# Kernel tuning notes

Hardware: AMD Instinct MI355X
Metric: run time of the kernel (lower is better)

## Reference

```python
import jax, jax.numpy as jnp
import numpy as np

B, N, NS, D, H = 32, 4096, 16, 512, 8
DH = D // H          # dims_per_head = 64
DFF = 4 * D          # ff_mlp hidden
SCALE = DH ** -0.5
EPS = 1e-8           # slot-attention renorm eps
LN_EPS = 1e-5        # torch LayerNorm default
ITERS = 3


def layer_norm(x, g, b):
    mu = jnp.mean(x, axis=-1, keepdims=True)
    var = jnp.mean((x - mu) ** 2, axis=-1, keepdims=True)
    return (x - mu) * jax.lax.rsqrt(var + LN_EPS) * g + b


def setup_inputs() -> dict:
    key = jax.random.key(0)
    ks = jax.random.split(key, 8)
    s = 0.02
    return {
        "inputs": jax.random.normal(ks[0], (B, N, D), jnp.float32),
        "conditioning": jax.random.normal(ks[1], (B, NS, D), jnp.float32),
        # norm_input
        "ln_in_g": jnp.ones((D,), jnp.float32),
        "ln_in_b": jnp.zeros((D,), jnp.float32),
        # projections (no bias: use_projection_bias=False)
        "Wk": jax.random.normal(ks[2], (D, D), jnp.float32) * s,
        "Wv": jax.random.normal(ks[3], (D, D), jnp.float32) * s,
        "Wq": jax.random.normal(ks[4], (D, D), jnp.float32) * s,
        "Wo": jax.random.normal(ks[5], (D, D), jnp.float32) * s,
        # norm_slots / norm_slots_ff_mlp
        "ln_s_g": jnp.ones((D,), jnp.float32),
        "ln_s_b": jnp.zeros((D,), jnp.float32),
        "ln_f_g": jnp.ones((D,), jnp.float32),
        "ln_f_b": jnp.zeros((D,), jnp.float32),
        # ff_mlp: Linear(D,4D) -> ReLU -> Linear(4D,D)
        "W1": jax.random.normal(ks[6], (D, DFF), jnp.float32) * s,
        "b1": jnp.zeros((DFF,), jnp.float32),
        "W2": jax.random.normal(ks[7], (DFF, D), jnp.float32) * s,
        "b2": jnp.zeros((D,), jnp.float32),
    }


def reference(inputs, conditioning, ln_in_g, ln_in_b, Wk, Wv, Wq, Wo,
              ln_s_g, ln_s_b, ln_f_g, ln_f_b, W1, b1, W2, b2):
    b = inputs.shape[0]
    x = layer_norm(inputs, ln_in_g, ln_in_b)                 # [b, n, D]
    k = (x @ Wk.T).reshape(b, N, H, DH)                      # [b, n, h, dh]
    v = (x @ Wv.T).reshape(b, N, H, DH)

    slots = conditioning
    attn_mean = None
    for _ in range(ITERS):
        slots_prev = slots
        s = layer_norm(slots, ln_s_g, ln_s_b)
        q = (s @ Wq.T).reshape(b, NS, H, DH)                 # [b, ns, h, dh]
        dots = jnp.einsum("bihd,bjhd->bihj", q, k) * SCALE   # [b, ns, h, n]
        # softmax over flattened (slots, heads) axis, per input location j
        attn = jax.nn.softmax(dots.reshape(b, NS * H, N), axis=1)
        attn = attn.reshape(b, NS, H, N)
        attn_before = attn
        attn = attn + EPS
        attn = attn / jnp.sum(attn, axis=-1, keepdims=True)  # renorm over j
        updates = jnp.einsum("bjhd,bihj->bihd", v, attn)     # [b, ns, h, dh]
        updates = updates.reshape(b, NS, D)
        slots = updates @ Wo.T + slots_prev                  # to_o + residual
        slots_prev_ff = slots
        s2 = layer_norm(slots, ln_f_g, ln_f_b)
        s2 = jax.nn.relu(s2 @ W1 + b1) @ W2 + b2             # ff_mlp
        slots = s2 + slots_prev_ff
        attn_mean = jnp.mean(attn_before, axis=2)            # [b, ns, n]
    return slots, attn_mean
```

## Files before the change

kernel.cpp:

```cpp
#include <hip/hip_runtime.h>
#include <cstdint>
#include <cstddef>

typedef __attribute__((ext_vector_type(8))) short short8;
typedef __attribute__((ext_vector_type(4))) short short4v;
typedef __attribute__((ext_vector_type(8))) __bf16 bf16x8;
typedef __attribute__((ext_vector_type(4))) float f32x4;
typedef unsigned short u16;

static constexpr int Bb = 32, Nn = 4096, NSs = 16, Dd = 512, Hh = 8, DFF = 2048;
static constexpr float SCALE = 0.125f;
static constexpr float EPSR  = 1e-8f;
static constexpr float LN_EPS = 1e-5f;
static constexpr int JS = 16;

__device__ __forceinline__ u16 f2b(float x) {
  union { float f; uint32_t u; } a; a.f = x;
  uint32_t r = a.u + 0x7fffu + ((a.u >> 16) & 1u);
  return (u16)(r >> 16);
}
__device__ __forceinline__ float b2f(u16 x) {
  union { uint32_t u; float f; } a; a.u = ((uint32_t)x) << 16; return a.f;
}

__device__ __forceinline__ f32x4 mfma16(short8 a, short8 b, f32x4 c) {
  return __builtin_amdgcn_mfma_f32_16x16x32_bf16(
      __builtin_bit_cast(bf16x8, a), __builtin_bit_cast(bf16x8, b), c, 0, 0, 0);
}

__device__ __forceinline__ void gload16(const u16* g, u16* l) {
  __builtin_amdgcn_global_load_lds(
      (const __attribute__((address_space(1))) void*)g,
      (__attribute__((address_space(3))) void*)l, 16, 0, 0);
}

__global__ __launch_bounds__(256) void ln_rows(const float* __restrict__ src,
    const float* __restrict__ g, const float* __restrict__ bt,
    u16* __restrict__ dst, int R) {
  int row = blockIdx.x * 4 + (threadIdx.x >> 6);
  if (row >= R) return;
  int lane = threadIdx.x & 63;
  const float* p = src + (size_t)row * Dd + lane * 8;
  float4 u0 = *(const float4*)p;
  float4 u1 = *(const float4*)(p + 4);
  float x[8] = {u0.x,u0.y,u0.z,u0.w,u1.x,u1.y,u1.z,u1.w};
  float s = 0.f, s2 = 0.f;
#pragma unroll
  for (int e = 0; e < 8; ++e) { s += x[e]; s2 += x[e]*x[e]; }
#pragma unroll
  for (int m = 1; m < 64; m <<= 1) { s += __shfl_xor(s, m); s2 += __shfl_xor(s2, m); }
  float mean = s * (1.f/512.f);
  float var  = s2 * (1.f/512.f) - mean*mean;
  float rstd = rsqrtf(var + LN_EPS);
  union { u16 o[8]; short8 v; } ou;
#pragma unroll
  for (int e = 0; e < 8; ++e)
    ou.o[e] = f2b((x[e]-mean)*rstd*g[lane*8+e] + bt[lane*8+e]);
  *(short8*)(dst + (size_t)row * Dd + lane * 8) = ou.v;
}

__global__ __launch_bounds__(256, 2) void gemm_kv(const u16* __restrict__ A,
    const u16* __restrict__ Bk, const u16* __restrict__ Bv,
    u16* __restrict__ Ck, u16* __restrict__ CvT) {
  __shared__ u16 lA[128*64];
  __shared__ u16 lK[128*64];
  __shared__ u16 lV[128*64];
  const int tid = threadIdx.x, lane = tid & 63, wid = tid >> 6;
  const int wr = wid >> 1, wc = wid & 1;
  const int n  = blockIdx.y * 4 + blockIdx.x;
  const int orig = (n & 7) * 512 + (n >> 3);
  const int bm = (orig >> 2) * 128, bn = (orig & 3) * 128;
  const size_t BN = (size_t)Bb * Nn;
  f32x4 ak[4][4] = {};
  f32x4 av[4][4] = {};
  const int sr = lane >> 3;
  const int ss = ((lane & 7) ^ (sr & 7)) * 8;
  const int li = lane & 15, lk = lane >> 4;
  const int sx = (li & 7) * 8;
  for (int t = 0; t < 8; ++t) {
    const int k0 = t * 64;
    __syncthreads();
#pragma unroll
    for (int gi = 0; gi < 4; ++gi) {
      const int rb = wid * 32 + gi * 8;
      gload16(A  + (size_t)(bm + rb + sr) * Dd + k0 + ss, &lA[rb * 64]);
      gload16(Bk + (size_t)(bn + rb + sr) * Dd + k0 + ss, &lK[rb * 64]);
      gload16(Bv + (size_t)(bn + rb + sr) * Dd + k0 + ss, &lV[rb * 64]);
    }
    __syncthreads();
#pragma unroll
    for (int kk = 0; kk < 2; ++kk) {
      const int cs = ((kk * 4 + lk) * 8) ^ sx;
      short8 af[4], kf[4], vf[4];
#pragma unroll
      for (int m = 0; m < 4; ++m)
        af[m] = *(const short8*)&lA[(wr*64 + m*16 + li)*64 + cs];
#pragma unroll
      for (int nn2 = 0; nn2 < 4; ++nn2) {
        kf[nn2] = *(const short8*)&lK[(wc*64 + nn2*16 + li)*64 + cs];
        vf[nn2] = *(const short8*)&lV[(wc*64 + nn2*16 + li)*64 + cs];
      }
#pragma unroll
      for (int m = 0; m < 4; ++m)
#pragma unroll
        for (int nn2 = 0; nn2 < 4; ++nn2) {
          ak[m][nn2] = mfma16(kf[nn2], af[m], ak[m][nn2]);
          av[m][nn2] = mfma16(af[m], vf[nn2], av[m][nn2]);
        }
    }
  }
#pragma unroll
  for (int m = 0; m < 4; ++m)
#pragma unroll
    for (int nn2 = 0; nn2 < 4; ++nn2) {
      {
        int row = bm + wr*64 + m*16 + li;
        int c0  = bn + wc*64 + nn2*16 + lk*4;
        f32x4 vk = ak[m][nn2];
        union { u16 o[4]; short4v v4; } ou;
#pragma unroll
        for (int r = 0; r < 4; ++r) ou.o[r] = f2b(vk[r]);
        *(short4v*)&Ck[(size_t)row * Dd + c0] = ou.v4;
      }
      {
        int col = bn + wc*64 + nn2*16 + li;
        int r0  = bm + wr*64 + m*16 + lk*4;
        f32x4 vv = av[m][nn2];
        union { u16 o[4]; short4v v4; } ou;
#pragma unroll
        for (int r = 0; r < 4; ++r) ou.o[r] = f2b(vv[r]);
        *(short4v*)&CvT[(size_t)col * BN + r0] = ou.v4;
      }
    }
}

template<int EP>
__global__ __launch_bounds__(256) void gemm64(const u16* __restrict__ A,
    const u16* __restrict__ Bw, void* __restrict__ Cp,
    const float* __restrict__ bias, const float* __restrict__ res,
    int N, int K) {
  const int lane = threadIdx.x & 63, wid = threadIdx.x >> 6;
  const int wr = wid >> 1, wc = wid & 1;
  const int bm = blockIdx.y * 64, bn = blockIdx.x * 64;
  const int li = lane & 15, lk = lane >> 4;
  f32x4 acc[2][2] = {};
  const u16* Ap = A  + (size_t)(bm + wr*32 + li) * K + lk*8;
  const u16* Bp = Bw + (size_t)(bn + wc*32 + li) * K + lk*8;
#pragma unroll 4
  for (int k0 = 0; k0 < K; k0 += 32) {
    short8 af[2], bf[2];
    af[0] = *(const short8*)(Ap + k0);
    af[1] = *(const short8*)(Ap + (size_t)16*K + k0);
    bf[0] = *(const short8*)(Bp + k0);
    bf[1] = *(const short8*)(Bp + (size_t)16*K + k0);
#pragma unroll
    for (int m = 0; m < 2; ++m)
#pragma unroll
      for (int nn2 = 0; nn2 < 2; ++nn2)
        acc[m][nn2] = mfma16(bf[nn2], af[m], acc[m][nn2]);
  }
#pragma unroll
  for (int m = 0; m < 2; ++m)
#pragma unroll
    for (int nn2 = 0; nn2 < 2; ++nn2) {
      int row = bm + wr*32 + m*16 + li;
      int c0  = bn + wc*32 + nn2*16 + lk*4;
      size_t off = (size_t)row * N + c0;
      f32x4 v = acc[m][nn2];
      if constexpr (EP == 0) {
        union { u16 o[4]; short4v v4; } ou;
#pragma unroll
        for (int r = 0; r < 4; ++r) ou.o[r] = f2b(v[r]);
        *(short4v*)&((u16*)Cp)[off] = ou.v4;
      } else if constexpr (EP == 1) {
        float4 rr = *(const float4*)&res[off];
        float4 o = {v[0] + rr.x, v[1] + rr.y, v[2] + rr.z, v[3] + rr.w};
        *(float4*)&((float*)Cp)[off] = o;
      } else if constexpr (EP == 2) {
        float4 bb = *(const float4*)&bias[c0];
        union { u16 o[4]; short4v v4; } ou;
        float x0 = v[0] + bb.x, x1 = v[1] + bb.y, x2 = v[2] + bb.z, x3 = v[3] + bb.w;
        ou.o[0] = f2b(x0 > 0.f ? x0 : 0.f); ou.o[1] = f2b(x1 > 0.f ? x1 : 0.f);
        ou.o[2] = f2b(x2 > 0.f ? x2 : 0.f); ou.o[3] = f2b(x3 > 0.f ? x3 : 0.f);
        *(short4v*)&((u16*)Cp)[off] = ou.v4;
      } else {
        float4 bb = *(const float4*)&bias[c0];
        float4 rr = *(const float4*)&res[off];
        float4 o = {v[0] + bb.x + rr.x, v[1] + bb.y + rr.y,
                    v[2] + bb.z + rr.z, v[3] + bb.w + rr.w};
        *(float4*)&((float*)Cp)[off] = o;
      }
    }
}

__global__ __launch_bounds__(512, 4) void attn_f(const u16* __restrict__ q,
    const u16* __restrict__ kk, const u16* __restrict__ vT,
    float* __restrict__ rowsum, float* __restrict__ Tpart,
    float* __restrict__ attn_mean) {
  const int js = blockIdx.x, b = blockIdx.y;
  const int tid = threadIdx.x, lane = tid & 63, h = tid >> 6;
  __shared__ float redM[8][64];
  __shared__ float redS[8][64];
  __shared__ u16 P2[8][16][72];
  const int li = lane & 15, lk = lane >> 4;
  const size_t BN = (size_t)Bb * Nn;
  const u16* qb = q + (((size_t)b*16 + li)*8 + h)*64 + lk*8;
  short8 a0 = *(const short8*)qb;
  short8 a1 = *(const short8*)(qb + 32);
  f32x4 apv[4] = {};
  float rs_acc[4] = {0.f, 0.f, 0.f, 0.f};
  for (int t2 = 0; t2 < 4; ++t2) {
    const int j0 = js * 256 + t2 * 64;
    f32x4 dt[4];
#pragma unroll
    for (int n = 0; n < 4; ++n) {
      const u16* kb = kk + ((size_t)b*Nn + j0 + n*16 + li)*Dd + h*64 + lk*8;
      f32x4 acc = {};
      acc = mfma16(a0, *(const short8*)kb, acc);
      acc = mfma16(a1, *(const short8*)(kb + 32), acc);
#pragma unroll
      for (int r = 0; r < 4; ++r) dt[n][r] = acc[r] * SCALE;
    }
#pragma unroll
    for (int n = 0; n < 4; ++n) {
      float v = fmaxf(fmaxf(dt[n][0], dt[n][1]), fmaxf(dt[n][2], dt[n][3]));
      v = fmaxf(v, __shfl_xor(v, 16));
      v = fmaxf(v, __shfl_xor(v, 32));
      if (lk == 0) redM[h][n*16 + li] = v;
    }
    __syncthreads();
    float M[4];
#pragma unroll
    for (int n = 0; n < 4; ++n) {
      float m2 = redM[0][n*16 + li];
#pragma unroll
      for (int p = 1; p < 8; ++p) m2 = fmaxf(m2, redM[p][n*16 + li]);
      M[n] = m2;
    }
#pragma unroll
    for (int n = 0; n < 4; ++n) {
      float s = 0.f;
#pragma unroll
      for (int r = 0; r < 4; ++r) { dt[n][r] = __expf(dt[n][r] - M[n]); s += dt[n][r]; }
      s += __shfl_xor(s, 16);
      s += __shfl_xor(s, 32);
      if (lk == 0) redS[h][n*16 + li] = s;
    }
    __syncthreads();
#pragma unroll
    for (int n = 0; n < 4; ++n) {
      float s2 = redS[0][n*16 + li];
#pragma unroll
      for (int p = 1; p < 8; ++p) s2 += redS[p][n*16 + li];
      float inv = 1.f / s2;
#pragma unroll
      for (int r = 0; r < 4; ++r) dt[n][r] = dt[n][r] * inv + EPSR;
    }
#pragma unroll
    for (int n = 0; n < 4; ++n)
#pragma unroll
      for (int r = 0; r < 4; ++r)
        P2[h][lk*4 + r][n*16 + li] = f2b(dt[n][r]);
#pragma unroll
    for (int r = 0; r < 4; ++r) {
      float v = dt[0][r] + dt[1][r] + dt[2][r] + dt[3][r];
      v += __shfl_xor(v, 1); v += __shfl_xor(v, 2);
      v += __shfl_xor(v, 4); v += __shfl_xor(v, 8);
      rs_acc[r] += v;
    }
    short8 pa0 = *(const short8*)&P2[h][li][lk*8];
    short8 pa1 = *(const short8*)&P2[h][li][32 + lk*8];
#pragma unroll
    for (int n = 0; n < 4; ++n) {
      const u16* vb = vT + (size_t)(h*64 + n*16 + li)*BN + (size_t)b*Nn + j0 + lk*8;
      apv[n] = mfma16(*(const short8*)vb, pa0, apv[n]);
      apv[n] = mfma16(*(const short8*)(vb + 32), pa1, apv[n]);
    }
    if (attn_mean != nullptr) {
      __syncthreads();
      int j = tid & 63;
#pragma unroll
      for (int ii = 0; ii < 2; ++ii) {
        int i = (tid >> 6) + ii*8;
        float sm = 0.f;
#pragma unroll
        for (int hh = 0; hh < 8; ++hh) sm += b2f(P2[hh][i][j]);
        attn_mean[((size_t)b*16 + i)*Nn + j0 + j] = sm * 0.125f - EPSR;
      }
      __syncthreads();
    }
  }
  float* Tout = Tpart + (((size_t)js * Bb + b) * 8 + h) * 16 * 64;
#pragma unroll
  for (int n = 0; n < 4; ++n) {
    float4 o = {apv[n][0], apv[n][1], apv[n][2], apv[n][3]};
    *(float4*)&Tout[(size_t)li * 64 + n*16 + lk*4] = o;
  }
  if (li == 0)
#pragma unroll
    for (int r = 0; r < 4; ++r)
      atomicAdd(&rowsum[b*128 + (lk*4 + r)*8 + h], rs_acc[r]);
}

__global__ void upd_c(const float* __restrict__ Tpart,
    const float* __restrict__ rs, u16* __restrict__ updb) {
  int idx = blockIdx.x * 256 + threadIdx.x;
  int o = idx & 511, bi = idx >> 9;
  int b = bi >> 4, i = bi & 15;
  int h = o >> 6, d = o & 63;
  size_t base = (((size_t)b * 8 + h) * 16 + i) * 64 + d;
  const size_t stride = (size_t)Bb * 8 * 16 * 64;
  float t = 0.f;
#pragma unroll
  for (int p = 0; p < JS; ++p) t += Tpart[base + p * stride];
  updb[idx] = f2b(t / rs[b * 128 + i * 8 + h]);
}

__global__ void cvt_w(const float* __restrict__ s, u16* __restrict__ d, int n) {
  int i = blockIdx.x*256 + threadIdx.x;
  if (i < n) d[i] = f2b(s[i]);
}
__global__ __launch_bounds__(256) void tr_cvt(const float* __restrict__ s,
    u16* __restrict__ d, int R, int C) {
  __shared__ u16 t[32][33];
  const int c0 = blockIdx.x*32, r0 = blockIdx.y*32;
  const int tr = threadIdx.x >> 3, tc4 = (threadIdx.x & 7)*4;
  float4 v = *(const float4*)&s[(size_t)(r0+tr)*C + c0 + tc4];
  t[tr][tc4+0] = f2b(v.x); t[tr][tc4+1] = f2b(v.y);
  t[tr][tc4+2] = f2b(v.z); t[tr][tc4+3] = f2b(v.w);
  __syncthreads();
  const int oc = threadIdx.x >> 3, or4 = (threadIdx.x & 7)*4;
  union { u16 o[4]; short4v v4; } ou;
#pragma unroll
  for (int e = 0; e < 4; ++e) ou.o[e] = t[or4+e][oc];
  *(short4v*)&d[(size_t)(c0+oc)*R + r0 + or4] = ou.v4;
}
__global__ void copy_f32v4(const float* __restrict__ s, float* __restrict__ d, int n4) {
  int i = blockIdx.x*256 + threadIdx.x;
  if (i < n4) ((float4*)d)[i] = ((const float4*)s)[i];
}

extern "C" void kernel_launch(void* const* d_in, const int* in_sizes, int n_in,
                              void* d_out, int out_size, void* d_ws, size_t ws_size,
                              hipStream_t stream) {
  (void)in_sizes; (void)n_in; (void)out_size; (void)ws_size;
  const float* inputs  = (const float*)d_in[0];
  const float* cond    = (const float*)d_in[1];
  const float* ln_in_g = (const float*)d_in[2];
  const float* ln_in_b = (const float*)d_in[3];
  const float* Wk = (const float*)d_in[4];
  const float* Wv = (const float*)d_in[5];
  const float* Wq = (const float*)d_in[6];
  const float* Wo = (const float*)d_in[7];
  const float* ln_s_g = (const float*)d_in[8];
  const float* ln_s_b = (const float*)d_in[9];
  const float* ln_f_g = (const float*)d_in[10];
  const float* ln_f_b = (const float*)d_in[11];
  const float* W1 = (const float*)d_in[12];
  const float* b1 = (const float*)d_in[13];
  const float* W2 = (const float*)d_in[14];
  const float* b2 = (const float*)d_in[15];
  float* out_slots = (float*)d_out;
  float* out_amean = (float*)d_out + (size_t)Bb*NSs*Dd;

  char* w = (char*)d_ws;
  auto alloc = [&](size_t bytes) {
    char* p = w; w += (bytes + 255) & ~(size_t)255; return p;
  };
  u16*  xn    = (u16*)alloc((size_t)Bb*Nn*Dd*2);
  u16*  kbuf  = (u16*)alloc((size_t)Bb*Nn*Dd*2);
  u16*  vT    = (u16*)alloc((size_t)Bb*Nn*Dd*2);
  float* Tpart = (float*)alloc((size_t)JS*Bb*8*16*64*4);
  float* slots = (float*)alloc((size_t)Bb*NSs*Dd*4);
  u16*  qb    = (u16*)alloc((size_t)Bb*NSs*Dd*2);
  u16*  snb   = (u16*)alloc((size_t)Bb*NSs*Dd*2);
  u16*  s2nb  = (u16*)alloc((size_t)Bb*NSs*Dd*2);
  u16*  h1b   = (u16*)alloc((size_t)Bb*NSs*DFF*2);
  u16*  updb  = (u16*)alloc((size_t)Bb*NSs*Dd*2);
  float* rowsum = (float*)alloc((size_t)Bb*128*3*4);
  u16*  wkb = (u16*)alloc(262144*2);
  u16*  wvb = (u16*)alloc(262144*2);
  u16*  wqb = (u16*)alloc(262144*2);
  u16*  wob = (u16*)alloc(262144*2);
  u16*  w1t = (u16*)alloc((size_t)1048576*2);
  u16*  w2t = (u16*)alloc((size_t)1048576*2);

  cvt_w<<<1024, 256, 0, stream>>>(Wk, wkb, 262144);
  cvt_w<<<1024, 256, 0, stream>>>(Wv, wvb, 262144);
  cvt_w<<<1024, 256, 0, stream>>>(Wq, wqb, 262144);
  cvt_w<<<1024, 256, 0, stream>>>(Wo, wob, 262144);
  tr_cvt<<<dim3(64, 16), 256, 0, stream>>>(W1, w1t, 512, 2048);
  tr_cvt<<<dim3(16, 64), 256, 0, stream>>>(W2, w2t, 2048, 512);
  copy_f32v4<<<256, 256, 0, stream>>>(cond, slots, 65536);
  (void)hipMemsetAsync(rowsum, 0, (size_t)Bb*128*3*4, stream);
  ln_rows<<<Bb*Nn/4, 256, 0, stream>>>(inputs, ln_in_g, ln_in_b, xn, Bb*Nn);
  gemm_kv<<<dim3(4, Bb*Nn/128), 256, 0, stream>>>(xn, wkb, wvb, kbuf, vT);

  for (int it = 0; it < 3; ++it) {
    float* rsp = rowsum + (size_t)it * Bb * 128;
    ln_rows<<<128, 256, 0, stream>>>(slots, ln_s_g, ln_s_b, snb, Bb*NSs);
    gemm64<0><<<dim3(8, 8), 256, 0, stream>>>(snb, wqb, qb, nullptr, nullptr, 512, 512);
    attn_f<<<dim3(JS, Bb), 512, 0, stream>>>(qb, kbuf, vT, rsp, Tpart,
                                             it == 2 ? out_amean : nullptr);
    upd_c<<<1024, 256, 0, stream>>>(Tpart, rsp, updb);
    gemm64<1><<<dim3(8, 8), 256, 0, stream>>>(updb, wob, slots, nullptr, slots, 512, 512);
    ln_rows<<<128, 256, 0, stream>>>(slots, ln_f_g, ln_f_b, s2nb, Bb*NSs);
    gemm64<2><<<dim3(32, 8), 256, 0, stream>>>(s2nb, w1t, h1b, b1, nullptr, 2048, 512);
    gemm64<3><<<dim3(8, 8), 256, 0, stream>>>(h1b, w2t, slots, b2, slots, 512, 2048);
  }
  copy_f32v4<<<256, 256, 0, stream>>>(slots, out_slots, 65536);
}
```

Before: 708.6 us.

## Double-buffer K/V projection GEMM with 256-row tiles and phased MFMA/load interleave

Rewrites the fused K/V projection GEMM to use 512-thread blocks with 256x128 tiles and double-buffered LDS. Global-to-LDS loads for the next k-step are issued in four slices between MFMA phases, with explicit barriers, waitcnts and setprio. The goal is to hide memory latency behind matrix math and reuse each A tile across more columns. LDS use roughly triples, which may limit occupancy to fewer blocks per CU, and the hand-placed waitcnt counts must exactly match the number of loads still in flight.

Result: no change. 700.3 us, median of 3 (-1.2%).

```diff
diff --git a/kernel.cpp b/kernel.cpp
--- a/kernel.cpp
+++ b/kernel.cpp
@@ -59,73 +59,163 @@
   *(short8*)(dst + (size_t)row * Dd + lane * 8) = ou.v;
 }
 
-__global__ __launch_bounds__(256, 2) void gemm_kv(const u16* __restrict__ A,
+__global__ __launch_bounds__(512, 2) void gemm_kv(const u16* __restrict__ A,
     const u16* __restrict__ Bk, const u16* __restrict__ Bv,
     u16* __restrict__ Ck, u16* __restrict__ CvT) {
-  __shared__ u16 lA[128*64];
-  __shared__ u16 lK[128*64];
-  __shared__ u16 lV[128*64];
+  __shared__ u16 lA[2][256*64];
+  __shared__ u16 lK[2][128*64];
+  __shared__ u16 lV[2][128*64];
   const int tid = threadIdx.x, lane = tid & 63, wid = tid >> 6;
-  const int wr = wid >> 1, wc = wid & 1;
-  const int n  = blockIdx.y * 4 + blockIdx.x;
-  const int orig = (n & 7) * 512 + (n >> 3);
-  const int bm = (orig >> 2) * 128, bn = (orig & 3) * 128;
+  const int wr = wid >> 2, wn = wid & 3;
+  const int n = blockIdx.x;
+  const int orig = (n & 7) * 256 + (n >> 3);
+  const int bm = (orig >> 2) * 256, bn = (orig & 3) * 128;
   const size_t BN = (size_t)Bb * Nn;
-  f32x4 ak[4][4] = {};
-  f32x4 av[4][4] = {};
+  f32x4 ak[8][2] = {};
+  f32x4 av[8][2] = {};
   const int sr = lane >> 3;
   const int ss = ((lane & 7) ^ (sr & 7)) * 8;
   const int li = lane & 15, lk = lane >> 4;
-  const int sx = (li & 7) * 8;
+#define STG_A(buf, tt, h) do { \
+    gload16(A + (size_t)(bm + (h)*128 + wid*16 + sr) * Dd + (tt)*64 + ss, \
+            &lA[buf][((h)*128 + wid*16) * 64]); \
+    gload16(A + (size_t)(bm + (h)*128 + wid*16 + 8 + sr) * Dd + (tt)*64 + ss, \
+            &lA[buf][((h)*128 + wid*16 + 8) * 64]); \
+  } while (0)
+#define STG_K(buf, tt) do { \
+    gload16(Bk + (size_t)(bn + wid*16 + sr) * Dd + (tt)*64 + ss, \
+            &lK[buf][(wid*16) * 64]); \
+    gload16(Bk + (size_t)(bn + wid*16 + 8 + sr) * Dd + (tt)*64 + ss, \
+            &lK[buf][(wid*16 + 8) * 64]); \
+  } while (0)
+#define STG_V(buf, tt) do { \
+    gload16(Bv + (size_t)(bn + wid*16 + sr) * Dd + (tt)*64 + ss, \
+            &lV[buf][(wid*16) * 64]); \
+    gload16(Bv + (size_t)(bn + wid*16 + 8 + sr) * Dd + (tt)*64 + ss, \
+            &lV[buf][(wid*16 + 8) * 64]); \
+  } while (0)
+#define PH_ENTER() do { \
+    __builtin_amdgcn_sched_barrier(0); \
+    __builtin_amdgcn_s_barrier(); \
+    asm volatile("s_waitcnt lgkmcnt(0)" ::: "memory"); \
+    __builtin_amdgcn_sched_barrier(0); \
+    __builtin_amdgcn_s_setprio(1); \
+  } while (0)
+#define PH_EXIT() do { \
+    __builtin_amdgcn_s_setprio(0); \
+    __builtin_amdgcn_sched_barrier(0); \
+    __builtin_amdgcn_s_barrier(); \
+    __builtin_amdgcn_sched_barrier(0); \
+  } while (0)
+#define PH_EXIT_VM(nvm) do { \
+    __builtin_amdgcn_s_setprio(0); \
+    __builtin_amdgcn_sched_barrier(0); \
+    if (nvm) asm volatile("s_waitcnt vmcnt(2)" ::: "memory"); \
+    else     asm volatile("s_waitcnt vmcnt(0)" ::: "memory"); \
+    __builtin_amdgcn_sched_barrier(0); \
+    __builtin_amdgcn_s_barrier(); \
+    __builtin_amdgcn_sched_barrier(0); \
+  } while (0)
+  STG_A(0, 0, 0);
+  STG_A(0, 0, 1);
+  STG_K(0, 0);
+  STG_V(0, 0);
+  asm volatile("s_waitcnt vmcnt(2)" ::: "memory");
+  __builtin_amdgcn_sched_barrier(0);
+  __builtin_amdgcn_s_barrier();
+  __builtin_amdgcn_sched_barrier(0);
   for (int t = 0; t < 8; ++t) {
-    const int k0 = t * 64;
-    __syncthreads();
-#pragma unroll
-    for (int gi = 0; gi < 4; ++gi) {
-      const int rb = wid * 32 + gi * 8;
-      gload16(A  + (size_t)(bm + rb + sr) * Dd + k0 + ss, &lA[rb * 64]);
-      gload16(Bk + (size_t)(bn + rb + sr) * Dd + k0 + ss, &lK[rb * 64]);
-      gload16(Bv + (size_t)(bn + rb + sr) * Dd + k0 + ss, &lV[rb * 64]);
-    }
-    __syncthreads();
-#pragma unroll
-    for (int kk = 0; kk < 2; ++kk) {
-      const int cs = ((kk * 4 + lk) * 8) ^ sx;
-      short8 af[4], kf[4], vf[4];
-#pragma unroll
-      for (int m = 0; m < 4; ++m)
-        af[m] = *(const short8*)&lA[(wr*64 + m*16 + li)*64 + cs];
-#pragma unroll
-      for (int nn2 = 0; nn2 < 4; ++nn2) {
-        kf[nn2] = *(const short8*)&lK[(wc*64 + nn2*16 + li)*64 + cs];
-        vf[nn2] = *(const short8*)&lV[(wc*64 + nn2*16 + li)*64 + cs];
-      }
-#pragma unroll
-      for (int m = 0; m < 4; ++m)
-#pragma unroll
-        for (int nn2 = 0; nn2 < 4; ++nn2) {
-          ak[m][nn2] = mfma16(kf[nn2], af[m], ak[m][nn2]);
-          av[m][nn2] = mfma16(af[m], vf[nn2], av[m][nn2]);
-        }
-    }
+    const int cb = t & 1, nb = cb ^ 1, tn = t + 1;
+    const bool nl = (t != 7);
+    short8 afA[4][2], afB[4][2], kf[2][2], vf[2][2];
+#pragma unroll
+    for (int m = 0; m < 4; ++m)
+#pragma unroll
+      for (int ks = 0; ks < 2; ++ks)
+        afA[m][ks] = *(const short8*)&lA[cb][(wr*128 + m*16 + li)*64
+                                            + (((ks*4 + lk) ^ (li & 7))*8)];
+#pragma unroll
+    for (int c = 0; c < 2; ++c)
+#pragma unroll
+      for (int ks = 0; ks < 2; ++ks)
+        kf[c][ks] = *(const short8*)&lK[cb][(wn*32 + c*16 + li)*64
+                                            + (((ks*4 + lk) ^ (li & 7))*8)];
+    if (nl) STG_A(nb, tn, 0);
+    PH_ENTER();
+#pragma unroll
+    for (int m = 0; m < 4; ++m)
+#pragma unroll
+      for (int c = 0; c < 2; ++c)
+#pragma unroll
+        for (int ks = 0; ks < 2; ++ks)
+          ak[m][c] = mfma16(kf[c][ks], afA[m][ks], ak[m][c]);
+    PH_EXIT_VM(nl);
+#pragma unroll
+    for (int c = 0; c < 2; ++c)
+#pragma unroll
+      for (int ks = 0; ks < 2; ++ks)
+        vf[c][ks] = *(const short8*)&lV[cb][(wn*32 + c*16 + li)*64
+                                            + (((ks*4 + lk) ^ (li & 7))*8)];
+    if (nl) STG_A(nb, tn, 1);
+    PH_ENTER();
+#pragma unroll
+    for (int m = 0; m < 4; ++m)
+#pragma unroll
+      for (int c = 0; c < 2; ++c)
+#pragma unroll
+        for (int ks = 0; ks < 2; ++ks)
+          av[m][c] = mfma16(afA[m][ks], vf[c][ks], av[m][c]);
+    PH_EXIT();
+#pragma unroll
+    for (int m = 0; m < 4; ++m)
+#pragma unroll
+      for (int ks = 0; ks < 2; ++ks)
+        afB[m][ks] = *(const short8*)&lA[cb][(wr*128 + (m + 4)*16 + li)*64
+                                            + (((ks*4 + lk) ^ (li & 7))*8)];
+    if (nl) STG_K(nb, tn);
+    PH_ENTER();
+#pragma unroll
+    for (int m = 0; m < 4; ++m)
+#pragma unroll
+      for (int c = 0; c < 2; ++c)
+#pragma unroll
+        for (int ks = 0; ks < 2; ++ks)
+          ak[m + 4][c] = mfma16(kf[c][ks], afB[m][ks], ak[m + 4][c]);
+    PH_EXIT();
+    if (nl) STG_V(nb, tn);
+    PH_ENTER();
+#pragma unroll
+    for (int m = 0; m < 4; ++m)
+#pragma unroll
+      for (int c = 0; c < 2; ++c)
+#pragma unroll
+        for (int ks = 0; ks < 2; ++ks)
+          av[m + 4][c] = mfma16(afB[m][ks], vf[c][ks], av[m + 4][c]);
+    PH_EXIT_VM(nl);
   }
-#pragma unroll
-  for (int m = 0; m < 4; ++m)
-#pragma unroll
-    for (int nn2 = 0; nn2 < 4; ++nn2) {
+#undef STG_A
+#undef STG_K
+#undef STG_V
+#undef PH_ENTER
+#undef PH_EXIT
+#undef PH_EXIT_VM
+#pragma unroll
+  for (int m = 0; m < 8; ++m)
+#pragma unroll
+    for (int c = 0; c < 2; ++c) {
       {
-        int row = bm + wr*64 + m*16 + li;
-        int c0  = bn + wc*64 + nn2*16 + lk*4;
-        f32x4 vk = ak[m][nn2];
+        int row = bm + wr*128 + m*16 + li;
+        int c0  = bn + wn*32 + c*16 + lk*4;
+        f32x4 vk = ak[m][c];
         union { u16 o[4]; short4v v4; } ou;
 #pragma unroll
         for (int r = 0; r < 4; ++r) ou.o[r] = f2b(vk[r]);
         *(short4v*)&Ck[(size_t)row * Dd + c0] = ou.v4;
       }
       {
-        int col = bn + wc*64 + nn2*16 + li;
-        int r0  = bm + wr*64 + m*16 + lk*4;
-        f32x4 vv = av[m][nn2];
+        int col = bn + wn*32 + c*16 + li;
+        int r0  = bm + wr*128 + m*16 + lk*4;
+        f32x4 vv = av[m][c];
         union { u16 o[4]; short4v v4; } ou;
 #pragma unroll
         for (int r = 0; r < 4; ++r) ou.o[r] = f2b(vv[r]);
@@ -394,7 +484,7 @@
   copy_f32v4<<<256, 256, 0, stream>>>(cond, slots, 65536);
   (void)hipMemsetAsync(rowsum, 0, (size_t)Bb*128*3*4, stream);
   ln_rows<<<Bb*Nn/4, 256, 0, stream>>>(inputs, ln_in_g, ln_in_b, xn, Bb*Nn);
-  gemm_kv<<<dim3(4, Bb*Nn/128), 256, 0, stream>>>(xn, wkb, wvb, kbuf, vT);
+  gemm_kv<<<2048, 512, 0, stream>>>(xn, wkb, wvb, kbuf, vT);
 
   for (int it = 0; it < 3; ++it) {
     float* rsp = rowsum + (size_t)it * Bb * 128;
```
